# Kernel tuning notes

Hardware: AMD Instinct MI355X
Metric: run time of the kernel (lower is better)

## Reference

```python
import jax, jax.numpy as jnp
import numpy as np

BN_EPS = 1e-5
W_SCALE = 0.04  # ~1/sqrt(h_dim), keeps gate pre-activations in a sane range


def setup_inputs() -> dict:
    key = jax.random.key(0)
    ks = jax.random.split(key, 5)
    B, T, K, X, H = 64, 256, 5, 512, 512
    x = jax.random.normal(ks[0], (B, T, K, X), dtype=jnp.float32)
    W_ih = jax.random.normal(ks[1], (4 * H, 2 * X), dtype=jnp.float32) * W_SCALE
    W_hh = jax.random.normal(ks[2], (4 * H, H), dtype=jnp.float32) * W_SCALE
    b_ih = jax.random.normal(ks[3], (4 * H,), dtype=jnp.float32) * W_SCALE
    b_hh = jax.random.normal(ks[4], (4 * H,), dtype=jnp.float32) * W_SCALE
    gamma = jnp.ones((T,), dtype=jnp.float32)   # BatchNorm1d(channels=T)
    beta = jnp.zeros((T,), dtype=jnp.float32)
    return {"x": x, "W_ih": W_ih, "W_hh": W_hh, "b_ih": b_ih, "b_hh": b_hh,
            "gamma": gamma, "beta": beta}


def _lstm_block(x, W_ih, W_hh, b_ih, b_hh, gamma, beta):
    B, T, K, X = x.shape
    H = W_hh.shape[1]
    # build LSTM input: source stream + mean of remaining streams, concat on features
    x_g_s = x[:, :, 0, :]                      # [B, T, X]
    x_g_r = jnp.mean(x[:, :, 1:, :], axis=2)   # [B, T, X]
    x_g_t = jnp.concatenate((x_g_s, x_g_r), axis=-1)

    # input projection for all timesteps at once: [B, T, 4H]
    pre = jnp.einsum('btf,gf->btg', x_g_t, W_ih) + (b_ih + b_hh)
    pre_t = jnp.transpose(pre, (1, 0, 2))      # [T, B, 4H] for scan

    def step(carry, p):
        h, c = carry
        z = p + h @ W_hh.T                     # [B, 4H]
        i, f, g, o = jnp.split(z, 4, axis=-1)  # torch gate order: i, f, g, o
        i = jax.nn.sigmoid(i)
        f = jax.nn.sigmoid(f)
        g = jnp.tanh(g)
        o = jax.nn.sigmoid(o)
        c = f * c + i * g
        h = o * jnp.tanh(c)
        return (h, c), h

    h0 = jnp.zeros((B, H), dtype=x.dtype)
    c0 = jnp.zeros((B, H), dtype=x.dtype)
    _, out_t = jax.lax.scan(step, (h0, c0), pre_t)   # [T, B, H]
    out = jnp.transpose(out_t, (1, 0, 2))            # [B, T, H]

    # BatchNorm1d over channel dim T (torch normalizes over batch and last dim)
    mean = jnp.mean(out, axis=(0, 2))                # [T]
    var = jnp.var(out, axis=(0, 2))                  # biased, per torch BN
    out = (out - mean[None, :, None]) * jax.lax.rsqrt(var + BN_EPS)[None, :, None]
    out = out * gamma[None, :, None] + beta[None, :, None]

    out = jax.nn.elu(out)
    return jnp.mean(out, axis=1)                     # [B, H]


def reference(x, W_ih, W_hh, b_ih, b_hh, gamma, beta):
    return _lstm_block(x, W_ih, W_hh, b_ih, b_hh, gamma, beta)
```

## Files before the change

kernel.cpp:

```cpp
#include <hip/hip_runtime.h>

typedef __attribute__((ext_vector_type(8))) short short8;
typedef __attribute__((ext_vector_type(4))) float floatx4;
typedef __attribute__((ext_vector_type(2))) float floatx2;

#define NBLK_SCAN 32

__device__ inline unsigned short f2bf(float x){
  unsigned u = __float_as_uint(x);
  u += 0x7FFFu + ((u >> 16) & 1u);
  return (unsigned short)(u >> 16);
}
__device__ inline int pk(float a, float b){
  return (int)f2bf(a) | ((int)f2bf(b) << 16);
}
__device__ inline float sigm(float x){ return 1.0f / (1.0f + __expf(-x)); }
__device__ inline float tanh_(float x){ return 1.0f - 2.0f / (__expf(2.0f*x) + 1.0f); }

__global__ void k_prep(const float* __restrict__ x, unsigned short* __restrict__ A){
  int c = blockIdx.x * 256 + threadIdx.x;
  int r = c >> 7;
  int fc = c & 127;
  int f = fc * 8;
  const float* xr = x + (size_t)r * 5 * 512;
  float v[8];
  if (f < 512){
    float4 a = *(const float4*)(xr + f);
    float4 b = *(const float4*)(xr + f + 4);
    v[0]=a.x; v[1]=a.y; v[2]=a.z; v[3]=a.w; v[4]=b.x; v[5]=b.y; v[6]=b.z; v[7]=b.w;
  } else {
    int fr = f - 512;
    #pragma unroll
    for (int j = 0; j < 8; ++j) v[j] = 0.f;
    #pragma unroll
    for (int k = 1; k <= 4; ++k){
      float4 a = *(const float4*)(xr + k*512 + fr);
      float4 b = *(const float4*)(xr + k*512 + fr + 4);
      v[0]+=a.x; v[1]+=a.y; v[2]+=a.z; v[3]+=a.w; v[4]+=b.x; v[5]+=b.y; v[6]+=b.z; v[7]+=b.w;
    }
    #pragma unroll
    for (int j = 0; j < 8; ++j) v[j] *= 0.25f;
  }
  int4 o;
  o.x = pk(v[0],v[1]); o.y = pk(v[2],v[3]); o.z = pk(v[4],v[5]); o.w = pk(v[6],v[7]);
  *(int4*)(A + (size_t)c * 8) = o;
}

__global__ void k_wcvt(const float* __restrict__ W, unsigned short* __restrict__ Wb){
  int c = blockIdx.x * 256 + threadIdx.x;
  const float* p = W + (size_t)c * 8;
  float4 a = *(const float4*)(p);
  float4 b = *(const float4*)(p + 4);
  int4 o;
  o.x = pk(a.x,a.y); o.y = pk(a.z,a.w); o.z = pk(b.x,b.y); o.w = pk(b.z,b.w);
  *(int4*)(Wb + (size_t)c * 8) = o;
}

__global__ void k_bias(const float* __restrict__ b_ih, const float* __restrict__ b_hh,
                       float* __restrict__ bias){
  int g = blockIdx.x * 256 + threadIdx.x;
  bias[g] = b_ih[g] + b_hh[g];
}

__launch_bounds__(256, 2)
__global__ void k_gemm(const unsigned short* __restrict__ A, const unsigned short* __restrict__ Wb,
                       const float* __restrict__ bias, float* __restrict__ pre){
  __shared__ unsigned short As[128*32];
  __shared__ unsigned short Bs[128*32];
  int tid = threadIdx.x;
  int bx = blockIdx.x;
  int by = blockIdx.y;
  int lane = tid & 63;
  int wid  = tid >> 6;
  int wm = wid >> 1, wn = wid & 1;
  int nn = lane & 15, q = lane >> 4;
  floatx4 acc[4][4] = {};

  int c1 = tid, c2 = tid + 256;
  const unsigned short* Ag = A  + (size_t)(by*128) * 1024;
  const unsigned short* Bg = Wb + (size_t)(bx*128) * 1024;

  for (int kb = 0; kb < 32; ++kb){
    if (kb) __syncthreads();
    {
      int4 va1 = *(const int4*)(Ag + (size_t)(c1>>2)*1024 + kb*32 + (c1&3)*8);
      int4 va2 = *(const int4*)(Ag + (size_t)(c2>>2)*1024 + kb*32 + (c2&3)*8);
      int4 vb1 = *(const int4*)(Bg + (size_t)(c1>>2)*1024 + kb*32 + (c1&3)*8);
      int4 vb2 = *(const int4*)(Bg + (size_t)(c2>>2)*1024 + kb*32 + (c2&3)*8);
      *(int4*)(As + c1*8) = va1; *(int4*)(As + c2*8) = va2;
      *(int4*)(Bs + c1*8) = vb1; *(int4*)(Bs + c2*8) = vb2;
    }
    __syncthreads();
    short8 a[4], b[4];
    #pragma unroll
    for (int mt = 0; mt < 4; ++mt)
      a[mt] = *(const short8*)(As + (wm*64 + mt*16 + nn)*32 + q*8);
    #pragma unroll
    for (int nt = 0; nt < 4; ++nt)
      b[nt] = *(const short8*)(Bs + (wn*64 + nt*16 + nn)*32 + q*8);
    #pragma unroll
    for (int mt = 0; mt < 4; ++mt)
      #pragma unroll
      for (int nt = 0; nt < 4; ++nt)
        acc[mt][nt] = __builtin_amdgcn_mfma_f32_16x16x32_bf16(a[mt], b[nt], acc[mt][nt], 0, 0, 0);
  }

  #pragma unroll
  for (int nt = 0; nt < 4; ++nt){
    int G = bx*128 + wn*64 + nt*16 + nn;
    float bv = bias[G];
    #pragma unroll
    for (int mt = 0; mt < 4; ++mt){
      #pragma unroll
      for (int r = 0; r < 4; ++r){
        int R = by*128 + wm*64 + mt*16 + q*4 + r;
        int b_ = R >> 8, t = R & 255;
        pre[(size_t)(t*64 + b_)*2048 + G] = acc[mt][nt][r] + bv;
      }
    }
  }
}

__launch_bounds__(256, 1)
__global__ void k_scan(const float* __restrict__ pre, const float* __restrict__ Whh,
                       int* __restrict__ h_buf,
                       float* __restrict__ out_t,
                       int* __restrict__ flags){
  extern __shared__ char smem[];
  short* h_s = (short*)smem;
  float* z_s = (float*)(smem + 64*520*2);

  int tid = threadIdx.x;
  int lane = tid & 63, w = tid >> 6;
  int nn = lane & 15, q = lane >> 4;
  int idx0 = blockIdx.x * 16;

  int cc = w*16 + nn;
  int il_b = cc >> 2, gate = cc & 3;
  const float* wr = Whh + (size_t)(gate*512 + idx0 + il_b) * 512;
  short8 Bf[16];
  #pragma unroll
  for (int kt = 0; kt < 16; ++kt){
    float4 f0 = *(const float4*)(wr + kt*32 + q*8);
    float4 f1 = *(const float4*)(wr + kt*32 + q*8 + 4);
    short8 bf;
    bf[0]=(short)f2bf(f0.x); bf[1]=(short)f2bf(f0.y); bf[2]=(short)f2bf(f0.z); bf[3]=(short)f2bf(f0.w);
    bf[4]=(short)f2bf(f1.x); bf[5]=(short)f2bf(f1.y); bf[6]=(short)f2bf(f1.z); bf[7]=(short)f2bf(f1.w);
    Bf[kt] = bf;
  }

  float cst[2][2] = {{0.f,0.f},{0.f,0.f}};

  for (int t = 0; t < 256; ++t){
    float2 pi[2], pf[2], pg[2], po[2];
    const float* pb = pre + (size_t)t * 64 * 2048;
    #pragma unroll
    for (int i = 0; i < 2; ++i){
      int p = tid + i*256; int b = p >> 3, il2 = p & 7;
      const float* bp = pb + (size_t)b*2048 + idx0 + il2*2;
      pi[i] = *(const float2*)(bp);
      pf[i] = *(const float2*)(bp + 512);
      pg[i] = *(const float2*)(bp + 1024);
      po[i] = *(const float2*)(bp + 1536);
    }

    if (t){
      if (tid < NBLK_SCAN){
        const int* fp = flags + tid*32;
        while (__hip_atomic_load(fp, __ATOMIC_ACQUIRE, __HIP_MEMORY_SCOPE_AGENT) < t)
          __builtin_amdgcn_s_sleep(1);
      }
      __syncthreads();
      const int* src = h_buf + ((t+1)&1)*16384;
      #pragma unroll
      for (int i = 0; i < 16; ++i){
        int c = tid + i*256;
        int b = c >> 6, ch = c & 63;
        const int* sp = src + c*4;
        int v0 = __hip_atomic_load(sp+0, __ATOMIC_RELAXED, __HIP_MEMORY_SCOPE_AGENT);
        int v1 = __hip_atomic_load(sp+1, __ATOMIC_RELAXED, __HIP_MEMORY_SCOPE_AGENT);
        int v2 = __hip_atomic_load(sp+2, __ATOMIC_RELAXED, __HIP_MEMORY_SCOPE_AGENT);
        int v3 = __hip_atomic_load(sp+3, __ATOMIC_RELAXED, __HIP_MEMORY_SCOPE_AGENT);
        int4 v; v.x=v0; v.y=v1; v.z=v2; v.w=v3;
        *(int4*)(h_s + b*520 + ch*8) = v;
      }
    } else {
      #pragma unroll
      for (int i = 0; i < 16; ++i){
        int c = tid + i*256; int b = c >> 6, ch = c & 63;
        int4 z4; z4.x=0; z4.y=0; z4.z=0; z4.w=0;
        *(int4*)(h_s + b*520 + ch*8) = z4;
      }
    }
    __syncthreads();

    floatx4 acc[4] = {};
    #pragma unroll
    for (int kt = 0; kt < 16; ++kt){
      short8 a[4];
      #pragma unroll
      for (int mt = 0; mt < 4; ++mt)
        a[mt] = *(const short8*)(h_s + (mt*16 + nn)*520 + kt*32 + q*8);
      #pragma unroll
      for (int mt = 0; mt < 4; ++mt)
        acc[mt] = __builtin_amdgcn_mfma_f32_16x16x32_bf16(a[mt], Bf[kt], acc[mt], 0, 0, 0);
    }

    #pragma unroll
    for (int mt = 0; mt < 4; ++mt)
      #pragma unroll
      for (int r = 0; r < 4; ++r)
        z_s[(mt*16 + q*4 + r)*68 + cc] = acc[mt][r];
    __syncthreads();

    int pbuf = t & 1;
    #pragma unroll
    for (int i = 0; i < 2; ++i){
      int p = tid + i*256; int b = p >> 3, il2 = p & 7;
      float4 za = *(const float4*)(z_s + b*68 + il2*8);
      float4 zb = *(const float4*)(z_s + b*68 + il2*8 + 4);
      float i0 = sigm(za.x + pi[i].x), f0 = sigm(za.y + pf[i].x);
      float g0 = tanh_(za.z + pg[i].x), o0 = sigm(za.w + po[i].x);
      float i1 = sigm(zb.x + pi[i].y), f1 = sigm(zb.y + pf[i].y);
      float g1 = tanh_(zb.z + pg[i].y), o1 = sigm(zb.w + po[i].y);
      float c0 = f0*cst[i][0] + i0*g0; cst[i][0] = c0;
      float c1 = f1*cst[i][1] + i1*g1; cst[i][1] = c1;
      float h0 = o0 * tanh_(c0);
      float h1 = o1 * tanh_(c1);
      floatx2 hv; hv.x = h0; hv.y = h1;
      __builtin_nontemporal_store(hv, (floatx2*)(out_t + ((size_t)t*64 + b)*512 + idx0 + il2*2));
      __hip_atomic_store(h_buf + pbuf*16384 + b*256 + (idx0>>1) + il2, pk(h0,h1),
                         __ATOMIC_RELAXED, __HIP_MEMORY_SCOPE_AGENT);
    }
    __syncthreads();
    if (tid == 0){
      __threadfence();
      __hip_atomic_store(flags + blockIdx.x*32, t+1,
                         __ATOMIC_RELEASE, __HIP_MEMORY_SCOPE_AGENT);
    }
  }
}

__global__ void k_stats(const float* __restrict__ out_t, float* __restrict__ mean_g,
                        float* __restrict__ rstd_g){
  int t = blockIdx.x, tid = threadIdx.x;
  const float4* p = (const float4*)(out_t + (size_t)t * 32768);
  float s = 0.f, s2 = 0.f;
  for (int i = tid; i < 8192; i += 256){
    float4 v = p[i];
    s  += v.x + v.y + v.z + v.w;
    s2 += v.x*v.x + v.y*v.y + v.z*v.z + v.w*v.w;
  }
  #pragma unroll
  for (int off = 32; off; off >>= 1){
    s  += __shfl_down(s, off, 64);
    s2 += __shfl_down(s2, off, 64);
  }
  __shared__ float red[8];
  int lane = tid & 63, wv = tid >> 6;
  if (lane == 0){ red[wv] = s; red[wv+4] = s2; }
  __syncthreads();
  if (tid == 0){
    float S  = red[0]+red[1]+red[2]+red[3];
    float S2 = red[4]+red[5]+red[6]+red[7];
    float m = S * (1.0f/32768.f);
    float var = S2 * (1.0f/32768.f) - m*m;
    mean_g[t] = m;
    rstd_g[t] = rsqrtf(var + 1e-5f);
  }
}

__global__ void k_final(const float* __restrict__ out_t, const float* __restrict__ mean_g,
                        const float* __restrict__ rstd_g, const float* __restrict__ gamma,
                        const float* __restrict__ beta, float* __restrict__ out){
  __shared__ float sm[1024];
  int tid = threadIdx.x;
  sm[tid]       = mean_g[tid];
  sm[256 + tid] = rstd_g[tid];
  sm[512 + tid] = gamma[tid];
  sm[768 + tid] = beta[tid];
  __syncthreads();
  int g = blockIdx.x * 256 + tid;
  float acc = 0.f;
  for (int t = 0; t < 256; ++t){
    float v = out_t[(size_t)t * 32768 + g];
    v = (v - sm[t]) * sm[256+t] * sm[512+t] + sm[768+t];
    acc += (v > 0.f) ? v : (__expf(v) - 1.0f);
  }
  out[g] = acc * (1.0f/256.0f);
}

extern "C" void kernel_launch(void* const* d_in, const int* in_sizes, int n_in,
                              void* d_out, int out_size, void* d_ws, size_t ws_size,
                              hipStream_t stream){
  const float* x     = (const float*)d_in[0];
  const float* W_ih  = (const float*)d_in[1];
  const float* W_hh  = (const float*)d_in[2];
  const float* b_ih  = (const float*)d_in[3];
  const float* b_hh  = (const float*)d_in[4];
  const float* gamma = (const float*)d_in[5];
  const float* beta  = (const float*)d_in[6];
  float* out = (float*)d_out;

  char* ws = (char*)d_ws;
  constexpr size_t OFF_PRE  = 33554432;
  constexpr size_t OFF_WB   = OFF_PRE + 134217728;
  constexpr size_t OFF_BIAS = OFF_WB + 4194304;
  constexpr size_t OFF_HG   = OFF_BIAS + 8192;
  constexpr size_t OFF_MEAN = OFF_HG + 65536;
  constexpr size_t OFF_RSTD = OFF_MEAN + 1024;
  constexpr size_t OFF_FLAG = OFF_RSTD + 1024;

  unsigned short* A    = (unsigned short*)ws;
  float* out_t         = (float*)ws;
  float* pre           = (float*)(ws + OFF_PRE);
  unsigned short* Wb   = (unsigned short*)(ws + OFF_WB);
  float* bias          = (float*)(ws + OFF_BIAS);
  int* h_buf           = (int*)(ws + OFF_HG);
  float* mean_g        = (float*)(ws + OFF_MEAN);
  float* rstd_g        = (float*)(ws + OFF_RSTD);
  int* flags           = (int*)(ws + OFF_FLAG);

  (void)hipMemsetAsync(flags, 0, NBLK_SCAN * 32 * sizeof(int), stream);
  k_prep<<<8192, 256, 0, stream>>>(x, A);
  k_wcvt<<<1024, 256, 0, stream>>>(W_ih, Wb);
  k_bias<<<8, 256, 0, stream>>>(b_ih, b_hh, bias);
  k_gemm<<<dim3(16, 128), 256, 0, stream>>>(A, Wb, bias, pre);
  k_scan<<<NBLK_SCAN, 256, 64*520*2 + 64*68*4, stream>>>(pre, W_hh, h_buf, out_t, flags);
  k_stats<<<256, 256, 0, stream>>>(out_t, mean_g, rstd_g);
  k_final<<<128, 256, 0, stream>>>(out_t, mean_g, rstd_g, gamma, beta, out);
}
```

Baseline: 2.834 ms.

## Switch to fp16 MFMA and per-producer fine-grained flag waits in LSTM scan

Changes the bf16 conversions and MFMAs to fp16 throughout the GEMM and scan. Restructures the recurrent hidden-state exchange so each producer block writes a contiguous slab, and each wavefront polls only its own producers' flags before copying that slab. This overlaps waiting with loading instead of using one block-wide barrier. It also drops the explicit threadfence before the release store and pads the LDS row stride to 530. The acquire is now only a signal fence after relaxed polling, which risks weaker memory ordering, and fp16 changes the numeric range.

```diff
diff --git a/kernel.cpp b/kernel.cpp
--- a/kernel.cpp
+++ b/kernel.cpp
@@ -1,18 +1,16 @@
 #include <hip/hip_runtime.h>
 
-typedef __attribute__((ext_vector_type(8))) short short8;
+typedef __attribute__((ext_vector_type(8))) _Float16 half8;
 typedef __attribute__((ext_vector_type(4))) float floatx4;
 typedef __attribute__((ext_vector_type(2))) float floatx2;
 
 #define NBLK_SCAN 32
 
-__device__ inline unsigned short f2bf(float x){
-  unsigned u = __float_as_uint(x);
-  u += 0x7FFFu + ((u >> 16) & 1u);
-  return (unsigned short)(u >> 16);
-}
-__device__ inline int pk(float a, float b){
-  return (int)f2bf(a) | ((int)f2bf(b) << 16);
+__device__ inline int pkh(float a, float b){
+  _Float16 ha = (_Float16)a, hb = (_Float16)b;
+  unsigned short ua = __builtin_bit_cast(unsigned short, ha);
+  unsigned short ub = __builtin_bit_cast(unsigned short, hb);
+  return (int)ua | ((int)ub << 16);
 }
 __device__ inline float sigm(float x){ return 1.0f / (1.0f + __expf(-x)); }
 __device__ inline float tanh_(float x){ return 1.0f - 2.0f / (__expf(2.0f*x) + 1.0f); }
@@ -42,7 +40,7 @@
     for (int j = 0; j < 8; ++j) v[j] *= 0.25f;
   }
   int4 o;
-  o.x = pk(v[0],v[1]); o.y = pk(v[2],v[3]); o.z = pk(v[4],v[5]); o.w = pk(v[6],v[7]);
+  o.x = pkh(v[0],v[1]); o.y = pkh(v[2],v[3]); o.z = pkh(v[4],v[5]); o.w = pkh(v[6],v[7]);
   *(int4*)(A + (size_t)c * 8) = o;
 }
 
@@ -52,7 +50,7 @@
   float4 a = *(const float4*)(p);
   float4 b = *(const float4*)(p + 4);
   int4 o;
-  o.x = pk(a.x,a.y); o.y = pk(a.z,a.w); o.z = pk(b.x,b.y); o.w = pk(b.z,b.w);
+  o.x = pkh(a.x,a.y); o.y = pkh(a.z,a.w); o.z = pkh(b.x,b.y); o.w = pkh(b.z,b.w);
   *(int4*)(Wb + (size_t)c * 8) = o;
 }
 
@@ -91,18 +89,18 @@
       *(int4*)(Bs + c1*8) = vb1; *(int4*)(Bs + c2*8) = vb2;
     }
     __syncthreads();
-    short8 a[4], b[4];
+    half8 a[4], b[4];
     #pragma unroll
     for (int mt = 0; mt < 4; ++mt)
-      a[mt] = *(const short8*)(As + (wm*64 + mt*16 + nn)*32 + q*8);
+      a[mt] = *(const half8*)(As + (wm*64 + mt*16 + nn)*32 + q*8);
     #pragma unroll
     for (int nt = 0; nt < 4; ++nt)
-      b[nt] = *(const short8*)(Bs + (wn*64 + nt*16 + nn)*32 + q*8);
+      b[nt] = *(const half8*)(Bs + (wn*64 + nt*16 + nn)*32 + q*8);
     #pragma unroll
     for (int mt = 0; mt < 4; ++mt)
       #pragma unroll
       for (int nt = 0; nt < 4; ++nt)
-        acc[mt][nt] = __builtin_amdgcn_mfma_f32_16x16x32_bf16(a[mt], b[nt], acc[mt][nt], 0, 0, 0);
+        acc[mt][nt] = __builtin_amdgcn_mfma_f32_16x16x32_f16(a[mt], b[nt], acc[mt][nt], 0, 0, 0);
   }
 
   #pragma unroll
@@ -123,12 +121,12 @@
 
 __launch_bounds__(256, 1)
 __global__ void k_scan(const float* __restrict__ pre, const float* __restrict__ Whh,
-                       int* __restrict__ h_buf,
+                       int* __restrict__ h_int,
                        float* __restrict__ out_t,
                        int* __restrict__ flags){
   extern __shared__ char smem[];
-  short* h_s = (short*)smem;
-  float* z_s = (float*)(smem + 64*520*2);
+  unsigned short* h_s = (unsigned short*)smem;
+  float* z_s = (float*)(smem + 64*530*2);
 
   int tid = threadIdx.x;
   int lane = tid & 63, w = tid >> 6;
@@ -138,14 +136,14 @@
   int cc = w*16 + nn;
   int il_b = cc >> 2, gate = cc & 3;
   const float* wr = Whh + (size_t)(gate*512 + idx0 + il_b) * 512;
-  short8 Bf[16];
+  half8 Bf[16];
   #pragma unroll
   for (int kt = 0; kt < 16; ++kt){
     float4 f0 = *(const float4*)(wr + kt*32 + q*8);
     float4 f1 = *(const float4*)(wr + kt*32 + q*8 + 4);
-    short8 bf;
-    bf[0]=(short)f2bf(f0.x); bf[1]=(short)f2bf(f0.y); bf[2]=(short)f2bf(f0.z); bf[3]=(short)f2bf(f0.w);
-    bf[4]=(short)f2bf(f1.x); bf[5]=(short)f2bf(f1.y); bf[6]=(short)f2bf(f1.z); bf[7]=(short)f2bf(f1.w);
+    half8 bf;
+    bf[0]=(_Float16)f0.x; bf[1]=(_Float16)f0.y; bf[2]=(_Float16)f0.z; bf[3]=(_Float16)f0.w;
+    bf[4]=(_Float16)f1.x; bf[5]=(_Float16)f1.y; bf[6]=(_Float16)f1.z; bf[7]=(_Float16)f1.w;
     Bf[kt] = bf;
   }
 
@@ -165,31 +163,42 @@
     }
 
     if (t){
-      if (tid < NBLK_SCAN){
-        const int* fp = flags + tid*32;
-        while (__hip_atomic_load(fp, __ATOMIC_ACQUIRE, __HIP_MEMORY_SCOPE_AGENT) < t)
-          __builtin_amdgcn_s_sleep(1);
-      }
-      __syncthreads();
-      const int* src = h_buf + ((t+1)&1)*16384;
-      #pragma unroll
-      for (int i = 0; i < 16; ++i){
-        int c = tid + i*256;
-        int b = c >> 6, ch = c & 63;
-        const int* sp = src + c*4;
+      const int* src = h_int + ((t+1)&1)*16384;
+      #pragma unroll
+      for (int jj = 0; jj < 8; ++jj){
+        int j = (jj<<2) | w;
+        int v = t;
+        if (lane == 0){
+          int* fp = flags + j*32;
+          while ((v = __hip_atomic_fetch_or(fp, 0, __ATOMIC_RELAXED, __HIP_MEMORY_SCOPE_AGENT)) < t)
+            __builtin_amdgcn_s_sleep(2);
+        }
+        v = __shfl(v, 0, 64);
+        __atomic_signal_fence(__ATOMIC_ACQUIRE);
+        (void)v;
+        const int* sp = src + j*512 + lane*8;
         int v0 = __hip_atomic_load(sp+0, __ATOMIC_RELAXED, __HIP_MEMORY_SCOPE_AGENT);
         int v1 = __hip_atomic_load(sp+1, __ATOMIC_RELAXED, __HIP_MEMORY_SCOPE_AGENT);
         int v2 = __hip_atomic_load(sp+2, __ATOMIC_RELAXED, __HIP_MEMORY_SCOPE_AGENT);
         int v3 = __hip_atomic_load(sp+3, __ATOMIC_RELAXED, __HIP_MEMORY_SCOPE_AGENT);
-        int4 v; v.x=v0; v.y=v1; v.z=v2; v.w=v3;
-        *(int4*)(h_s + b*520 + ch*8) = v;
+        int v4 = __hip_atomic_load(sp+4, __ATOMIC_RELAXED, __HIP_MEMORY_SCOPE_AGENT);
+        int v5 = __hip_atomic_load(sp+5, __ATOMIC_RELAXED, __HIP_MEMORY_SCOPE_AGENT);
+        int v6 = __hip_atomic_load(sp+6, __ATOMIC_RELAXED, __HIP_MEMORY_SCOPE_AGENT);
+        int v7 = __hip_atomic_load(sp+7, __ATOMIC_RELAXED, __HIP_MEMORY_SCOPE_AGENT);
+        int4 x0; x0.x=v0; x0.y=v1; x0.z=v2; x0.w=v3;
+        int4 x1; x1.x=v4; x1.y=v5; x1.z=v6; x1.w=v7;
+        unsigned short* dst = h_s + lane*530 + j*16;
+        *(int4*)(dst) = x0;
+        *(int4*)(dst + 8) = x1;
       }
     } else {
-      #pragma unroll
-      for (int i = 0; i < 16; ++i){
-        int c = tid + i*256; int b = c >> 6, ch = c & 63;
-        int4 z4; z4.x=0; z4.y=0; z4.z=0; z4.w=0;
-        *(int4*)(h_s + b*520 + ch*8) = z4;
+      int4 z4; z4.x=0; z4.y=0; z4.z=0; z4.w=0;
+      #pragma unroll
+      for (int jj = 0; jj < 8; ++jj){
+        int j = (jj<<2) | w;
+        unsigned short* dst = h_s + lane*530 + j*16;
+        *(int4*)(dst) = z4;
+        *(int4*)(dst + 8) = z4;
       }
     }
     __syncthreads();
@@ -197,13 +206,13 @@
     floatx4 acc[4] = {};
     #pragma unroll
     for (int kt = 0; kt < 16; ++kt){
-      short8 a[4];
+      half8 a[4];
       #pragma unroll
       for (int mt = 0; mt < 4; ++mt)
-        a[mt] = *(const short8*)(h_s + (mt*16 + nn)*520 + kt*32 + q*8);
+        a[mt] = *(const half8*)(h_s + (mt*16 + nn)*530 + kt*32 + q*8);
       #pragma unroll
       for (int mt = 0; mt < 4; ++mt)
-        acc[mt] = __builtin_amdgcn_mfma_f32_16x16x32_bf16(a[mt], Bf[kt], acc[mt], 0, 0, 0);
+        acc[mt] = __builtin_amdgcn_mfma_f32_16x16x32_f16(a[mt], Bf[kt], acc[mt], 0, 0, 0);
     }
 
     #pragma unroll
@@ -213,7 +222,7 @@
         z_s[(mt*16 + q*4 + r)*68 + cc] = acc[mt][r];
     __syncthreads();
 
-    int pbuf = t & 1;
+    int pbase = (t&1)*16384 + blockIdx.x*512;
     #pragma unroll
     for (int i = 0; i < 2; ++i){
       int p = tid + i*256; int b = p >> 3, il2 = p & 7;
@@ -229,15 +238,13 @@
       float h1 = o1 * tanh_(c1);
       floatx2 hv; hv.x = h0; hv.y = h1;
       __builtin_nontemporal_store(hv, (floatx2*)(out_t + ((size_t)t*64 + b)*512 + idx0 + il2*2));
-      __hip_atomic_store(h_buf + pbuf*16384 + b*256 + (idx0>>1) + il2, pk(h0,h1),
+      __hip_atomic_store(h_int + pbase + b*8 + il2, pkh(h0,h1),
                          __ATOMIC_RELAXED, __HIP_MEMORY_SCOPE_AGENT);
     }
     __syncthreads();
-    if (tid == 0){
-      __threadfence();
+    if (tid == 0)
       __hip_atomic_store(flags + blockIdx.x*32, t+1,
                          __ATOMIC_RELEASE, __HIP_MEMORY_SCOPE_AGENT);
-    }
   }
 }
 
@@ -307,7 +314,7 @@
   constexpr size_t OFF_WB   = OFF_PRE + 134217728;
   constexpr size_t OFF_BIAS = OFF_WB + 4194304;
   constexpr size_t OFF_HG   = OFF_BIAS + 8192;
-  constexpr size_t OFF_MEAN = OFF_HG + 65536;
+  constexpr size_t OFF_MEAN = OFF_HG + 131072;
   constexpr size_t OFF_RSTD = OFF_MEAN + 1024;
   constexpr size_t OFF_FLAG = OFF_RSTD + 1024;
 
@@ -316,7 +323,7 @@
   float* pre           = (float*)(ws + OFF_PRE);
   unsigned short* Wb   = (unsigned short*)(ws + OFF_WB);
   float* bias          = (float*)(ws + OFF_BIAS);
-  int* h_buf           = (int*)(ws + OFF_HG);
+  int* h_int           = (int*)(ws + OFF_HG);
   float* mean_g        = (float*)(ws + OFF_MEAN);
   float* rstd_g        = (float*)(ws + OFF_RSTD);
   int* flags           = (int*)(ws + OFF_FLAG);
@@ -326,7 +333,7 @@
   k_wcvt<<<1024, 256, 0, stream>>>(W_ih, Wb);
   k_bias<<<8, 256, 0, stream>>>(b_ih, b_hh, bias);
   k_gemm<<<dim3(16, 128), 256, 0, stream>>>(A, Wb, bias, pre);
-  k_scan<<<NBLK_SCAN, 256, 64*520*2 + 64*68*4, stream>>>(pre, W_hh, h_buf, out_t, flags);
+  k_scan<<<NBLK_SCAN, 256, 64*530*2 + 64*68*4, stream>>>(pre, W_hh, h_int, out_t, flags);
   k_stats<<<256, 256, 0, stream>>>(out_t, mean_g, rstd_g);
   k_final<<<128, 256, 0, stream>>>(out_t, mean_g, rstd_g, gamma, beta, out);
 }
```

After: 5.014 ms. 1.77x slower.
